# Performance work log

Hardware: AMD Instinct MI355X
Metric: run time of the kernel (lower is better)

Reference implementation:

```python
import jax, jax.numpy as jnp
import numpy as np

N_NODES = 50000
N_EDGES = 800000
IN_CH, HID_CH, OUT_CH = 256, 128, 64


def setup_inputs() -> dict:
    key = jax.random.key(0)
    k1, k2, k3, k4 = jax.random.split(key, 4)
    x = jax.random.normal(k1, (N_NODES, IN_CH), dtype=jnp.float32)
    edge_index = jax.random.randint(k2, (2, N_EDGES), 0, N_NODES, dtype=jnp.int64)
    # Glorot-style init for the GCN weight matrices, zero bias (PyG default)
    W1 = jax.random.normal(k3, (IN_CH, HID_CH), dtype=jnp.float32) * (1.0 / np.sqrt(IN_CH))
    b1 = jnp.zeros((HID_CH,), dtype=jnp.float32)
    W2 = jax.random.normal(k4, (HID_CH, OUT_CH), dtype=jnp.float32) * (1.0 / np.sqrt(HID_CH))
    b2 = jnp.zeros((OUT_CH,), dtype=jnp.float32)
    return {"x": x, "edge_index": edge_index, "W1": W1, "b1": b1, "W2": W2, "b2": b2}


def _gcn_conv(x, W, b, src, dst, dinv_sqrt, n_nodes):
    # linear transform then degree-normalized scatter-add aggregation
    h = x @ W                                        # [N, F_out]
    norm = dinv_sqrt[src] * dinv_sqrt[dst]           # [E+N]
    msg = h[src] * norm[:, None]                     # gather + scale
    out = jax.ops.segment_sum(msg, dst, num_segments=n_nodes)
    return out + b


def reference(x, edge_index, W1, b1, W2, b2):
    n_nodes = x.shape[0]
    loops = jnp.arange(n_nodes, dtype=edge_index.dtype)
    src = jnp.concatenate([edge_index[0], loops])    # add self-loops (PyG default)
    dst = jnp.concatenate([edge_index[1], loops])
    # symmetric normalization: deg computed over targets incl. self-loops
    deg = jax.ops.segment_sum(jnp.ones_like(dst, dtype=x.dtype), dst, num_segments=n_nodes)
    dinv_sqrt = jnp.where(deg > 0, jax.lax.rsqrt(deg), 0.0)
    h = jax.nn.relu(_gcn_conv(x, W1, b1, src, dst, dinv_sqrt, n_nodes))
    return _gcn_conv(h, W2, b2, src, dst, dinv_sqrt, n_nodes)
```

## Files before the change

### kernel.cpp

```cpp
#include <hip/hip_runtime.h>


typedef __attribute__((ext_vector_type(4))) float floatx4;
typedef _Float16 __attribute__((ext_vector_type(8))) half8v;

#define BUCK_SH 6
#define BUCK    64
#define NBLK    256

#define AS1(p) ((const __attribute__((address_space(1))) void*)(p))
#define AS3(p) ((__attribute__((address_space(3))) void*)(p))

__global__ void detect64_kernel(const int* __restrict__ ei, int* __restrict__ flag) {
    __shared__ int nz;
    if (threadIdx.x == 0) nz = 0;
    __syncthreads();
    if (ei[2 * threadIdx.x + 1] != 0) atomicOr(&nz, 1);
    __syncthreads();
    if (threadIdx.x == 0) *flag = (nz == 0) ? 1 : 0;
}

__device__ __forceinline__ int edge_id(const int* __restrict__ ei, int is64, long long pos) {
    return is64 ? ei[2 * pos] : ei[(int)pos];
}

__global__ void hist2_kernel(const int* __restrict__ ei, const int* __restrict__ flag,
                             int* __restrict__ hist2, int E, int NB, int chunk) {
    __shared__ int h[1024];
    const int t = threadIdx.x;
    for (int i = t; i < NB; i += blockDim.x) h[i] = 0;
    __syncthreads();
    const int is64 = *flag;
    const int lo = blockIdx.x * chunk;
    const int hi = min(E, lo + chunk);
    for (int e = lo + t; e < hi; e += blockDim.x) {
        int d = edge_id(ei, is64, (long long)E + e);
        atomicAdd(&h[d >> BUCK_SH], 1);
    }
    __syncthreads();
    for (int i = t; i < NB; i += blockDim.x) hist2[(long long)blockIdx.x * NB + i] = h[i];
}

__global__ void colscan_kernel(const int* __restrict__ hist2, int* __restrict__ start2t,
                               int* __restrict__ colsum, int NB) {
    int t = blockIdx.x * blockDim.x + threadIdx.x;
    if (t >= NB) return;
    int run = 0;
    for (int b = 0; b < NBLK; ++b) {
        int v = hist2[(long long)b * NB + t];
        start2t[(long long)t * NBLK + b] = run;
        run += v;
    }
    colsum[t] = run;
}

__global__ void basescan_kernel(const int* __restrict__ colsum, int* __restrict__ bbase,
                                int NB, int E) {
    __shared__ int sm[1024];
    const int t = threadIdx.x;
    int v = (t < NB) ? colsum[t] : 0;
    sm[t] = v;
    __syncthreads();
    for (int s = 1; s < 1024; s <<= 1) {
        int u = (t >= s) ? sm[t - s] : 0;
        __syncthreads();
        sm[t] += u;
        __syncthreads();
    }
    if (t < NB) bbase[t] = sm[t] - v;
    if (t == 0) bbase[NB] = E;
}

__global__ void scatter2_kernel(const int* __restrict__ ei, const int* __restrict__ flag,
                                const int* __restrict__ bbase, const int* __restrict__ start2t,
                                unsigned* __restrict__ ebuf, int E, int NB, int chunk) {
    __shared__ int hcur[1024];
    const int t = threadIdx.x;
    for (int i = t; i < NB; i += blockDim.x)
        hcur[i] = bbase[i] + start2t[(long long)i * NBLK + blockIdx.x];
    __syncthreads();
    const int is64 = *flag;
    const int lo = blockIdx.x * chunk;
    const int hi = min(E, lo + chunk);
    for (int e = lo + t; e < hi; e += blockDim.x) {
        int s = edge_id(ei, is64, e);
        int d = edge_id(ei, is64, (long long)E + e);
        int pos = atomicAdd(&hcur[d >> BUCK_SH], 1);
        ebuf[pos] = (unsigned)s | ((unsigned)(d & (BUCK - 1)) << 26);
    }
}

__global__ void csrbuild_kernel(const unsigned* __restrict__ ebuf, const int* __restrict__ bbase,
                                int* __restrict__ offs, float* __restrict__ dinv,
                                int* __restrict__ csr, int N, int NB, int E) {
    __shared__ int cnt[BUCK], exc[BUCK], cur[BUCK];
    const int b = blockIdx.x;
    const int t = threadIdx.x;
    if (t < BUCK) { cnt[t] = 0; cur[t] = 0; }
    __syncthreads();
    const int lo = bbase[b], hi = bbase[b + 1];
    for (int i = lo + t; i < hi; i += blockDim.x)
        atomicAdd(&cnt[ebuf[i] >> 26], 1);
    __syncthreads();
    if (t == 0) {
        int run = 0;
        for (int l = 0; l < BUCK; ++l) { exc[l] = run; run += cnt[l]; }
    }
    __syncthreads();
    if (t < BUCK) {
        int n = b * BUCK + t;
        if (n < N) {
            offs[n] = lo + exc[t];
            dinv[n] = rsqrtf(1.0f + (float)cnt[t]);
        }
    }
    if (b == NB - 1 && t == 0) offs[N] = E;
    for (int i = lo + t; i < hi; i += blockDim.x) {
        unsigned e = ebuf[i];
        int l = e >> 26;
        int p = lo + exc[l] + atomicAdd(&cur[l], 1);
        csr[p] = (int)(e & 0x03FFFFFFu);
    }
}

__device__ __forceinline__ void convW_one(const float* W, _Float16* Wt, int K, int Nc, int idx) {
    if (idx >= K * Nc) return;
    int k = idx / Nc, n = idx % Nc;
    Wt[(long long)n * K + k] = (_Float16)W[idx];
}

__global__ void convW_kernel(const float* __restrict__ W1, _Float16* __restrict__ T1,
                             int K1, int N1, int nb1,
                             const float* __restrict__ W2, _Float16* __restrict__ T2,
                             int K2, int N2) {
    if ((int)blockIdx.x < nb1) {
        convW_one(W1, T1, K1, N1, blockIdx.x * blockDim.x + threadIdx.x);
    } else {
        convW_one(W2, T2, K2, N2, (blockIdx.x - nb1) * blockDim.x + threadIdx.x);
    }
}

template <int NCOL, int K>
__launch_bounds__(256)
__global__ void gemm_f16_kernel(const float* __restrict__ A,
                                const _Float16* __restrict__ Bt,
                                _Float16* __restrict__ C, int M) {
    constexpr int NCB = NCOL / 16;
    constexpr int BM = 128, BK = 64;
    constexpr int NC = K / BK;
    constexpr int UNITS = BM * BK / 4;
    __shared__ float As[2][BM * BK];

    const int tid  = threadIdx.x;
    const int wave = tid >> 6;
    const int lane = tid & 63;
    const int n15  = lane & 15;
    const int q    = lane >> 4;
    const int row0 = blockIdx.x * BM;

    floatx4 acc[2][NCB];
#pragma unroll
    for (int rt = 0; rt < 2; ++rt)
#pragma unroll
        for (int c = 0; c < NCB; ++c) acc[rt][c] = (floatx4){0.f, 0.f, 0.f, 0.f};

    auto stage = [&](int buf, int kc) {
#pragma unroll
        for (int j = 0; j < UNITS / 256; ++j) {
            int g = j * 256 + tid;
            int r = g >> 4;
            int u = (g & 15) ^ (r & 15);
            int gr = row0 + r;
            if (gr >= M) gr = M - 1;
            const float* gp = &A[(long long)gr * K + kc + u * 4];
            float* lp = &As[buf][g * 4];
            __builtin_amdgcn_global_load_lds(AS1(gp), AS3(lp), 16, 0, 0);
        }
    };

    stage(0, 0);
    __syncthreads();

#pragma unroll
    for (int c = 0; c < NC; ++c) {
        if (c + 1 < NC) stage((c + 1) & 1, (c + 1) * BK);
        const int buf = c & 1;
#pragma unroll
        for (int ks = 0; ks < 2; ++ks) {
            half8v af[2];
#pragma unroll
            for (int rt = 0; rt < 2; ++rt) {
                const int R = wave * 32 + rt * 16 + n15;
                const int u0 = ks * 8 + q * 2;
                const int p0 = (u0)     ^ (R & 15);
                const int p1 = (u0 + 1) ^ (R & 15);
                float4 f0 = *(const float4*)&As[buf][R * BK + p0 * 4];
                float4 f1 = *(const float4*)&As[buf][R * BK + p1 * 4];
                af[rt][0] = (_Float16)f0.x; af[rt][1] = (_Float16)f0.y;
                af[rt][2] = (_Float16)f0.z; af[rt][3] = (_Float16)f0.w;
                af[rt][4] = (_Float16)f1.x; af[rt][5] = (_Float16)f1.y;
                af[rt][6] = (_Float16)f1.z; af[rt][7] = (_Float16)f1.w;
            }
#pragma unroll
            for (int cb = 0; cb < NCB; ++cb) {
                const _Float16* bp = &Bt[(long long)(cb * 16 + n15) * K + c * BK + ks * 32 + q * 8];
                half8v bf = *(const half8v*)bp;
                acc[0][cb] = __builtin_amdgcn_mfma_f32_16x16x32_f16(af[0], bf, acc[0][cb], 0, 0, 0);
                acc[1][cb] = __builtin_amdgcn_mfma_f32_16x16x32_f16(af[1], bf, acc[1][cb], 0, 0, 0);
            }
        }
        if (c + 1 < NC) __syncthreads();
    }

#pragma unroll
    for (int rt = 0; rt < 2; ++rt) {
#pragma unroll
        for (int cb = 0; cb < NCB; ++cb) {
            int col = cb * 16 + n15;
#pragma unroll
            for (int r = 0; r < 4; ++r) {
                int gr = row0 + wave * 32 + rt * 16 + q * 4 + r;
                if (gr < M) C[(long long)gr * NCOL + col] = (_Float16)acc[rt][cb][r];
            }
        }
    }
}

template <int F, int RELU>
__launch_bounds__(256)
__global__ void gatherh_kernel(const _Float16* __restrict__ h, const int* __restrict__ csr,
                               const int* __restrict__ offs, const float* __restrict__ dinv,
                               const float* __restrict__ bias, float* __restrict__ out, int N) {
    constexpr int L = F / 8;
    constexpr int NPB = 256 / L;
    const int n = blockIdx.x * NPB + threadIdx.x / L;
    const int c8 = (threadIdx.x % L) * 8;
    if (n >= N) return;

    const float di = dinv[n];
    half8v hs = *(const half8v*)&h[(long long)n * F + c8];
    float acc[8];
    const float sd = di * di;
#pragma unroll
    for (int j = 0; j < 8; ++j) acc[j] = (float)hs[j] * sd;

    const int end = offs[n + 1];
    for (int j = offs[n]; j < end; j += 8) {
        int s[8];
        float ws[8];
        half8v v[8];
#pragma unroll
        for (int u = 0; u < 8; ++u) {
            int jj = j + u;
            s[u] = csr[jj < end ? jj : end - 1];
        }
#pragma unroll
        for (int u = 0; u < 8; ++u)
            ws[u] = (j + u < end) ? dinv[s[u]] * di : 0.f;
#pragma unroll
        for (int u = 0; u < 8; ++u) v[u] = *(const half8v*)&h[(long long)s[u] * F + c8];
#pragma unroll
        for (int u = 0; u < 8; ++u) {
#pragma unroll
            for (int t = 0; t < 8; ++t) acc[t] = fmaf((float)v[u][t], ws[u], acc[t]);
        }
    }

    float4 b0 = *(const float4*)&bias[c8];
    float4 b1 = *(const float4*)&bias[c8 + 4];
    float bb[8] = {b0.x, b0.y, b0.z, b0.w, b1.x, b1.y, b1.z, b1.w};
#pragma unroll
    for (int t = 0; t < 8; ++t) {
        acc[t] += bb[t];
        if (RELU) acc[t] = fmaxf(acc[t], 0.f);
    }
    float* o = &out[(long long)n * F + c8];
    *(float4*)o       = make_float4(acc[0], acc[1], acc[2], acc[3]);
    *(float4*)(o + 4) = make_float4(acc[4], acc[5], acc[6], acc[7]);
}

extern "C" void kernel_launch(void* const* d_in, const int* in_sizes, int n_in,
                              void* d_out, int out_size, void* d_ws, size_t ws_size,
                              hipStream_t stream) {
    const float* x  = (const float*)d_in[0];
    const int*   ei = (const int*)d_in[1];
    const float* W1 = (const float*)d_in[2];
    const float* b1 = (const float*)d_in[3];
    const float* W2 = (const float*)d_in[4];
    const float* b2 = (const float*)d_in[5];
    float* out = (float*)d_out;

    const int IN_CH = 256, HID = 128, OUT = 64;
    const int N = in_sizes[0] / IN_CH;
    const int E = in_sizes[1] / 2;
    const int NB = (N + BUCK - 1) / BUCK;
    const int chunk = (E + NBLK - 1) / NBLK;

    char* w = (char*)d_ws;
    size_t off_b = 0;
    auto alloc = [&](size_t bytes) { void* p = w + off_b; off_b = (off_b + bytes + 255) & ~(size_t)255; return p; };
    int*   flag    = (int*)alloc(256);
    int*   hist2   = (int*)alloc((size_t)NBLK * NB * 4);
    int*   start2t = (int*)alloc((size_t)NB * NBLK * 4);
    int*   colsum  = (int*)alloc((size_t)NB * 4);
    int*   bbase   = (int*)alloc((size_t)(NB + 1) * 4);
    int*   offs    = (int*)alloc((size_t)(N + 1) * 4);
    float* dinv    = (float*)alloc((size_t)N * 4);
    unsigned* ebuf = (unsigned*)alloc((size_t)E * 4);
    int*   csr     = (int*)alloc((size_t)E * 4);
    _Float16* W1t  = (_Float16*)alloc((size_t)IN_CH * HID * 2);
    _Float16* W2t  = (_Float16*)alloc((size_t)HID * OUT * 2);
    _Float16* h1   = (_Float16*)alloc((size_t)N * HID * 2);
    float* agg1    = (float*)alloc((size_t)N * HID * 4);
    _Float16* h2   = h1;

    const int T = 256;
    detect64_kernel<<<1, 256, 0, stream>>>(ei, flag);
    hist2_kernel<<<NBLK, T, 0, stream>>>(ei, flag, hist2, E, NB, chunk);
    colscan_kernel<<<(NB + T - 1) / T, T, 0, stream>>>(hist2, start2t, colsum, NB);
    basescan_kernel<<<1, 1024, 0, stream>>>(colsum, bbase, NB, E);
    scatter2_kernel<<<NBLK, T, 0, stream>>>(ei, flag, bbase, start2t, ebuf, E, NB, chunk);
    csrbuild_kernel<<<NB, T, 0, stream>>>(ebuf, bbase, offs, dinv, csr, N, NB, E);

    {
        int nb1 = (IN_CH * HID + T - 1) / T;
        int nb2 = (HID * OUT + T - 1) / T;
        convW_kernel<<<nb1 + nb2, T, 0, stream>>>(W1, W1t, IN_CH, HID, nb1,
                                                  W2, W2t, HID, OUT);
    }

    gemm_f16_kernel<128, 256><<<(N + 127) / 128, 256, 0, stream>>>(x, W1t, h1, N);
    gatherh_kernel<128, 1><<<(N * 16 + 255) / 256, 256, 0, stream>>>(h1, csr, offs, dinv, b1, agg1, N);
    gemm_f16_kernel<64, 128><<<(N + 127) / 128, 256, 0, stream>>>(agg1, W2t, h2, N);
    gatherh_kernel<64, 0><<<(N * 8 + 255) / 256, 256, 0, stream>>>(h2, csr, offs, dinv, b2, out, N);
}
```

Measured before the change: 240.6 us.

## Fuse CSR preprocessing kernels into one cooperative kernel with grid syncs

Replaces the seven preprocessing launches (64-bit index detection, histogram, column scan, base scan, scatter, CSR build, weight conversion) with a single cooperative kernel of 256 blocks that separates the phases with grid.sync(). The aim is to remove per-launch overhead and the idle gaps between the small kernels. The cost is that the CSR build now runs on only 256 blocks, each looping over many buckets instead of one block per bucket, and the base scan runs on a single block while the rest of the grid waits. The original multi-kernel path is kept as a fallback if the cooperative launch fails.

Measured after the change: 424.2 us. +76.3%, slower.

```diff
diff --git a/kernel.cpp b/kernel.cpp
--- a/kernel.cpp
+++ b/kernel.cpp
@@ -1,4 +1,7 @@
 #include <hip/hip_runtime.h>
+#include <hip/hip_cooperative_groups.h>
+
+namespace cg = cooperative_groups;
 
 
 typedef __attribute__((ext_vector_type(4))) float floatx4;
@@ -11,6 +14,145 @@
 #define AS1(p) ((const __attribute__((address_space(1))) void*)(p))
 #define AS3(p) ((__attribute__((address_space(3))) void*)(p))
 
+__device__ __forceinline__ int edge_id(const int* __restrict__ ei, int is64, long long pos) {
+    return is64 ? ei[2 * pos] : ei[(int)pos];
+}
+
+__device__ __forceinline__ void convW_one(const float* W, _Float16* Wt, int K, int Nc, int idx) {
+    if (idx >= K * Nc) return;
+    int k = idx / Nc, n = idx % Nc;
+    Wt[(long long)n * K + k] = (_Float16)W[idx];
+}
+
+struct PrepParams {
+    const int* ei;
+    int E, NB, chunk, N;
+    int* hist2;
+    int* start2t;
+    int* colsum;
+    int* bbase;
+    unsigned* ebuf;
+    int* offs;
+    float* dinv;
+    int* csr;
+    const float* W1; _Float16* W1t;
+    const float* W2; _Float16* W2t;
+};
+
+__global__ void __launch_bounds__(256) prep_kernel(PrepParams p) {
+    cg::grid_group grid = cg::this_grid();
+    __shared__ int sh[1024];
+    __shared__ int cnt[BUCK], exc[BUCK], cur[BUCK];
+    __shared__ int shflag;
+    const int t = threadIdx.x;
+    const int b = blockIdx.x;
+
+    if (t == 0) shflag = 0;
+    __syncthreads();
+    if (p.ei[2 * t + 1] != 0) atomicOr(&shflag, 1);
+    __syncthreads();
+    const int is64 = (shflag == 0) ? 1 : 0;
+
+    const int lo = b * p.chunk;
+    const int hi = min(p.E, lo + p.chunk);
+
+    for (int i = t; i < p.NB; i += 256) sh[i] = 0;
+    __syncthreads();
+    for (int e = lo + t; e < hi; e += 256) {
+        int d = edge_id(p.ei, is64, (long long)p.E + e);
+        atomicAdd(&sh[d >> BUCK_SH], 1);
+    }
+    __syncthreads();
+    for (int i = t; i < p.NB; i += 256) p.hist2[(long long)b * p.NB + i] = sh[i];
+    {
+        int gtid = b * 256 + t;
+        convW_one(p.W1, p.W1t, 256, 128, gtid);
+        int g2 = gtid - 256 * 128;
+        if (g2 >= 0) convW_one(p.W2, p.W2t, 128, 64, g2);
+    }
+    grid.sync();
+
+    {
+        int gtid = b * 256 + t;
+        if (gtid < p.NB) {
+            int run = 0;
+            for (int b2 = 0; b2 < NBLK; ++b2) {
+                int v = p.hist2[(long long)b2 * p.NB + gtid];
+                p.start2t[(long long)gtid * NBLK + b2] = run;
+                run += v;
+            }
+            p.colsum[gtid] = run;
+        }
+    }
+    grid.sync();
+
+    if (b == 0) {
+        const int C = (p.NB + 255) / 256;
+        int vals[8];
+        int mysum = 0;
+        for (int i = 0; i < C; ++i) {
+            int idx = t * C + i;
+            int v = (idx < p.NB) ? p.colsum[idx] : 0;
+            vals[i] = v; mysum += v;
+        }
+        sh[t] = mysum;
+        __syncthreads();
+        for (int s = 1; s < 256; s <<= 1) {
+            int u = (t >= s) ? sh[t - s] : 0;
+            __syncthreads();
+            sh[t] += u;
+            __syncthreads();
+        }
+        int run = sh[t] - mysum;
+        for (int i = 0; i < C; ++i) {
+            int idx = t * C + i;
+            if (idx < p.NB) { p.bbase[idx] = run; run += vals[i]; }
+        }
+        if (t == 0) p.bbase[p.NB] = p.E;
+    }
+    grid.sync();
+
+    for (int i = t; i < p.NB; i += 256)
+        sh[i] = p.bbase[i] + p.start2t[(long long)i * NBLK + b];
+    __syncthreads();
+    for (int e = lo + t; e < hi; e += 256) {
+        int s = edge_id(p.ei, is64, e);
+        int d = edge_id(p.ei, is64, (long long)p.E + e);
+        int pos = atomicAdd(&sh[d >> BUCK_SH], 1);
+        p.ebuf[pos] = (unsigned)s | ((unsigned)(d & (BUCK - 1)) << 26);
+    }
+    grid.sync();
+
+    for (int bk = b; bk < p.NB; bk += NBLK) {
+        if (t < BUCK) { cnt[t] = 0; cur[t] = 0; }
+        __syncthreads();
+        const int l0 = p.bbase[bk], h0 = p.bbase[bk + 1];
+        for (int i = l0 + t; i < h0; i += 256)
+            atomicAdd(&cnt[p.ebuf[i] >> 26], 1);
+        __syncthreads();
+        if (t == 0) {
+            int run = 0;
+            for (int l = 0; l < BUCK; ++l) { exc[l] = run; run += cnt[l]; }
+        }
+        __syncthreads();
+        if (t < BUCK) {
+            int n = bk * BUCK + t;
+            if (n < p.N) {
+                p.offs[n] = l0 + exc[t];
+                p.dinv[n] = rsqrtf(1.0f + (float)cnt[t]);
+            }
+        }
+        if (bk == p.NB - 1 && t == 0) p.offs[p.N] = p.E;
+        for (int i = l0 + t; i < h0; i += 256) {
+            unsigned e = p.ebuf[i];
+            int l = e >> 26;
+            int pq = l0 + exc[l] + atomicAdd(&cur[l], 1);
+            p.csr[pq] = (int)(e & 0x03FFFFFFu);
+        }
+        __syncthreads();
+    }
+}
+
 __global__ void detect64_kernel(const int* __restrict__ ei, int* __restrict__ flag) {
     __shared__ int nz;
     if (threadIdx.x == 0) nz = 0;
@@ -18,10 +160,6 @@
     if (ei[2 * threadIdx.x + 1] != 0) atomicOr(&nz, 1);
     __syncthreads();
     if (threadIdx.x == 0) *flag = (nz == 0) ? 1 : 0;
-}
-
-__device__ __forceinline__ int edge_id(const int* __restrict__ ei, int is64, long long pos) {
-    return is64 ? ei[2 * pos] : ei[(int)pos];
 }
 
 __global__ void hist2_kernel(const int* __restrict__ ei, const int* __restrict__ flag,
@@ -121,12 +259,6 @@
         int p = lo + exc[l] + atomicAdd(&cur[l], 1);
         csr[p] = (int)(e & 0x03FFFFFFu);
     }
-}
-
-__device__ __forceinline__ void convW_one(const float* W, _Float16* Wt, int K, int Nc, int idx) {
-    if (idx >= K * Nc) return;
-    int k = idx / Nc, n = idx % Nc;
-    Wt[(long long)n * K + k] = (_Float16)W[idx];
 }
 
 __global__ void convW_kernel(const float* __restrict__ W1, _Float16* __restrict__ T1,
@@ -315,14 +447,22 @@
     _Float16* h2   = h1;
 
     const int T = 256;
-    detect64_kernel<<<1, 256, 0, stream>>>(ei, flag);
-    hist2_kernel<<<NBLK, T, 0, stream>>>(ei, flag, hist2, E, NB, chunk);
-    colscan_kernel<<<(NB + T - 1) / T, T, 0, stream>>>(hist2, start2t, colsum, NB);
-    basescan_kernel<<<1, 1024, 0, stream>>>(colsum, bbase, NB, E);
-    scatter2_kernel<<<NBLK, T, 0, stream>>>(ei, flag, bbase, start2t, ebuf, E, NB, chunk);
-    csrbuild_kernel<<<NB, T, 0, stream>>>(ebuf, bbase, offs, dinv, csr, N, NB, E);
-
-    {
+
+    PrepParams pp;
+    pp.ei = ei; pp.E = E; pp.NB = NB; pp.chunk = chunk; pp.N = N;
+    pp.hist2 = hist2; pp.start2t = start2t; pp.colsum = colsum; pp.bbase = bbase;
+    pp.ebuf = ebuf; pp.offs = offs; pp.dinv = dinv; pp.csr = csr;
+    pp.W1 = W1; pp.W1t = W1t; pp.W2 = W2; pp.W2t = W2t;
+    void* args[] = { &pp };
+    hipError_t cerr = hipLaunchCooperativeKernel((const void*)prep_kernel,
+                                                 dim3(NBLK), dim3(256), args, 0, stream);
+    if (cerr != hipSuccess) {
+        detect64_kernel<<<1, 256, 0, stream>>>(ei, flag);
+        hist2_kernel<<<NBLK, T, 0, stream>>>(ei, flag, hist2, E, NB, chunk);
+        colscan_kernel<<<(NB + T - 1) / T, T, 0, stream>>>(hist2, start2t, colsum, NB);
+        basescan_kernel<<<1, 1024, 0, stream>>>(colsum, bbase, NB, E);
+        scatter2_kernel<<<NBLK, T, 0, stream>>>(ei, flag, bbase, start2t, ebuf, E, NB, chunk);
+        csrbuild_kernel<<<NB, T, 0, stream>>>(ebuf, bbase, offs, dinv, csr, N, NB, E);
         int nb1 = (IN_CH * HID + T - 1) / T;
         int nb2 = (HID * OUT + T - 1) / T;
         convW_kernel<<<nb1 + nb2, T, 0, stream>>>(W1, W1t, IN_CH, HID, nb1,
```
